# Kernel tuning notes

Hardware: AMD Instinct MI355X
Metric: run time of the kernel (lower is better)

## Reference

```python
import jax, jax.numpy as jnp
import numpy as np

EPS = 1e-8  # torch F.cosine_similarity default eps


def _cos_gram(x):
    # row-normalize with eps-clamped norms, then Gram matrix [N, N]
    norms = jnp.maximum(jnp.linalg.norm(x, axis=1, keepdims=True), EPS)
    xn = x / norms
    return xn @ xn.T


def setup_inputs() -> dict:
    key = jax.random.key(0)
    k1, k2 = jax.random.split(key)
    N, D = 8192, 128
    return {
        "feat_q": jax.random.normal(k1, (N, D), dtype=jnp.float32),
        "feat_k": jax.random.normal(k2, (N, D), dtype=jnp.float32),
    }


def reference(feat_q, feat_k):
    feat_k = jax.lax.stop_gradient(feat_k)  # feat_k.detach()
    N = feat_q.shape[0]
    qsim = _cos_gram(feat_q)  # [N, N]
    ksim = _cos_gram(feat_k)  # [N, N]
    # mean of (qsim - ksim)^2 over all off-diagonal (i != j) pairs
    diff2 = (qsim - ksim) ** 2
    off_diag = ~jnp.eye(N, dtype=bool)
    denom = jnp.asarray(N * (N - 1), dtype=diff2.dtype)
    loss = jnp.sum(jnp.where(off_diag, diff2, 0.0)) / denom
    return loss
```

## Files before the change

kernel.cpp:

```cpp
#include <hip/hip_runtime.h>
#include <hip/hip_bf16.h>

#define NROWS 8192
#define DDIM  128
#define KTOT  256
#define GT_ROWB (NROWS * 2)
#define NKCH  64
#define CHN   (NROWS / NKCH)
#define NPAIR 10
#define GB_BLOCKS 160
#define LDSPAD 260

typedef unsigned short ushort_t;
typedef unsigned int   uint_t;
typedef __attribute__((ext_vector_type(8))) short short8;
typedef __attribute__((ext_vector_type(4))) float floatx4;

#define LDS_PTR(p) ((__attribute__((address_space(3))) void*)(p))
#define GLB_PTR(p) ((const __attribute__((address_space(1))) void*)(p))

static __device__ inline ushort_t f2bf(float f) {
    union { float f; uint_t u; } a; a.f = f;
    uint_t u = a.u + 0x7fffu + ((a.u >> 16) & 1u);
    return (ushort_t)(u >> 16);
}

static __device__ inline void pair_decode(int p, int* ti, int* tj) {
    int i = 0, len = 4;
    while (p >= len) { p -= len; len--; i++; }
    *ti = i; *tj = i + p;
}

__global__ __launch_bounds__(256) void norm_t_kernel(
    const float* __restrict__ q, const float* __restrict__ k,
    ushort_t* __restrict__ Gt, double* acc, uint_t* counter)
{
    __shared__ ushort_t lds[64 * LDSPAD];
    if (blockIdx.x == 0 && threadIdx.x == 0) { *acc = 0.0; *counter = 0u; }
    int w  = threadIdx.x >> 6;
    int l  = threadIdx.x & 63;
    int h  = l >> 5;
    int li = l & 31;

    #pragma unroll
    for (int i = 0; i < 8; ++i) {
        int rl  = w * 16 + 2 * i + h;
        int row = blockIdx.x * 64 + rl;
        {
            float4 v = ((const float4*)(q + (size_t)row * DDIM))[li];
            float ss = v.x * v.x + v.y * v.y + v.z * v.z + v.w * v.w;
            #pragma unroll
            for (int o = 16; o > 0; o >>= 1) ss += __shfl_xor(ss, o, 64);
            float inv = rsqrtf(fmaxf(ss, 1e-16f));
            uint2 p2;
            p2.x = (uint_t)f2bf(v.x * inv) | ((uint_t)f2bf(v.y * inv) << 16);
            p2.y = (uint_t)f2bf(v.z * inv) | ((uint_t)f2bf(v.w * inv) << 16);
            *(uint2*)&lds[rl * LDSPAD + 4 * li] = p2;
        }
        {
            float4 v = ((const float4*)(k + (size_t)row * DDIM))[li];
            float ss = v.x * v.x + v.y * v.y + v.z * v.z + v.w * v.w;
            #pragma unroll
            for (int o = 16; o > 0; o >>= 1) ss += __shfl_xor(ss, o, 64);
            float inv = rsqrtf(fmaxf(ss, 1e-16f));
            uint2 p2;
            p2.x = (uint_t)f2bf(v.x * inv) | ((uint_t)f2bf(v.y * inv) << 16);
            p2.y = (uint_t)f2bf(v.z * inv) | ((uint_t)f2bf(v.w * inv) << 16);
            *(uint2*)&lds[rl * LDSPAD + 128 + 4 * li] = p2;
        }
    }
    __syncthreads();

    int a = threadIdx.x;
    char* gdst = (char*)Gt + (size_t)a * GT_ROWB + (size_t)blockIdx.x * 128;
    #pragma unroll
    for (int g = 0; g < 8; ++g) {
        union { ushort_t u16[8]; uint4 v; } tmp;
        #pragma unroll
        for (int e = 0; e < 8; ++e)
            tmp.u16[e] = lds[(g * 8 + e) * LDSPAD + a];
        *(uint4*)(gdst + g * 16) = tmp.v;
    }
}

__global__ __launch_bounds__(128, 2) void gram_a_kernel(
    const ushort_t* __restrict__ Gt, float* __restrict__ P)
{
    __shared__ ushort_t sA[64 * CHN];
    __shared__ ushort_t sB[64 * CHN];

    int pair = blockIdx.x >> 6;
    int c    = blockIdx.x & 63;
    int ti, tj;
    pair_decode(pair, &ti, &tj);
    int tid = threadIdx.x;

    const char* gA = (const char*)Gt + (size_t)(ti * 64) * GT_ROWB + c * (CHN * 2);
    const char* gB = (const char*)Gt + (size_t)(tj * 64) * GT_ROWB + c * (CHN * 2);

    #pragma unroll
    for (int it = 0; it < 8; ++it) {
        int ch = it * 128 + tid;
        int row = ch >> 4, phys = ch & 15;
        int logical = phys ^ (row & 7);
        __builtin_amdgcn_global_load_lds(GLB_PTR(gA + (size_t)row * GT_ROWB + logical * 16),
                                         LDS_PTR((char*)sA + ch * 16), 16, 0, 0);
    }
    #pragma unroll
    for (int it = 0; it < 8; ++it) {
        int ch = it * 128 + tid;
        int row = ch >> 4, phys = ch & 15;
        int logical = phys ^ (row & 7);
        __builtin_amdgcn_global_load_lds(GLB_PTR(gB + (size_t)row * GT_ROWB + logical * 16),
                                         LDS_PTR((char*)sB + ch * 16), 16, 0, 0);
    }
    __syncthreads();

    int w    = tid >> 6;
    int l    = tid & 63;
    int m    = l & 15;
    int quad = l >> 4;

    floatx4 accC[2][4];
    #pragma unroll
    for (int at = 0; at < 2; ++at)
        #pragma unroll
        for (int bt = 0; bt < 4; ++bt)
            accC[at][bt] = (floatx4){0.f, 0.f, 0.f, 0.f};

    #pragma unroll
    for (int kp = 0; kp < 4; ++kp) {
        short8 af[2], bf[4];
        #pragma unroll
        for (int at = 0; at < 2; ++at) {
            int ra   = w * 32 + at * 16 + m;
            int phys = (kp * 4 + quad) ^ (ra & 7);
            af[at] = *(const short8*)&sA[ra * CHN + phys * 8];
        }
        #pragma unroll
        for (int bt = 0; bt < 4; ++bt) {
            int rb   = bt * 16 + m;
            int phys = (kp * 4 + quad) ^ (rb & 7);
            bf[bt] = *(const short8*)&sB[rb * CHN + phys * 8];
        }
        #pragma unroll
        for (int at = 0; at < 2; ++at)
            #pragma unroll
            for (int bt = 0; bt < 4; ++bt)
                accC[at][bt] = __builtin_amdgcn_mfma_f32_16x16x32_bf16(af[at], bf[bt], accC[at][bt], 0, 0, 0);
    }

    float* pt = P + ((size_t)pair * NKCH + c) * 4096;
    #pragma unroll
    for (int at = 0; at < 2; ++at)
        #pragma unroll
        for (int bt = 0; bt < 4; ++bt)
            #pragma unroll
            for (int r = 0; r < 4; ++r) {
                int row = w * 32 + at * 16 + quad * 4 + r;
                int col = bt * 16 + m;
                pt[row * 64 + col] = accC[at][bt][r];
            }
}

__global__ __launch_bounds__(256) void gram_b_kernel(
    const float* __restrict__ P, double* acc, uint_t* counter, float* out)
{
    __shared__ float wsum[4];
    int e    = blockIdx.x * 256 + threadIdx.x;
    int pair = e >> 12;
    int idx  = e & 4095;

    float s = 0.f;
    #pragma unroll
    for (int c = 0; c < NKCH; ++c)
        s += P[((size_t)pair * NKCH + c) * 4096 + idx];

    int ti, tj;
    pair_decode(pair, &ti, &tj);
    float wgt = ((ti < 2) == (tj < 2)) ? 1.f : -1.f;
    if (ti != tj) wgt *= 2.f;
    float v = wgt * s * s;

    int w = threadIdx.x >> 6, l = threadIdx.x & 63;
    #pragma unroll
    for (int o = 32; o > 0; o >>= 1) v += __shfl_xor(v, o, 64);
    if (l == 0) wsum[w] = v;
    __syncthreads();
    if (threadIdx.x == 0) {
        double t = (double)wsum[0] + (double)wsum[1] + (double)wsum[2] + (double)wsum[3];
        atomicAdd(acc, t);
        __threadfence();
        uint_t old = atomicAdd(counter, 1u);
        if (old == GB_BLOCKS - 1) {
            double total = atomicAdd(acc, 0.0);
            out[0] = (float)(total * (1.0 / ((double)NROWS * (double)(NROWS - 1))));
        }
    }
}

extern "C" void kernel_launch(void* const* d_in, const int* in_sizes, int n_in,
                              void* d_out, int out_size, void* d_ws, size_t ws_size,
                              hipStream_t stream) {
    const float* q = (const float*)d_in[0];
    const float* k = (const float*)d_in[1];
    float* out = (float*)d_out;

    double*   acc = (double*)d_ws;
    uint_t*   cnt = (uint_t*)((char*)d_ws + 64);
    ushort_t* Gt  = (ushort_t*)((char*)d_ws + 256);
    float*    P   = (float*)((char*)d_ws + 256 + (size_t)KTOT * GT_ROWB);

    norm_t_kernel<<<NROWS / 64, 256, 0, stream>>>(q, k, Gt, acc, cnt);
    gram_a_kernel<<<NPAIR * NKCH, 128, 0, stream>>>(Gt, P);
    gram_b_kernel<<<GB_BLOCKS, 256, 0, stream>>>(P, acc, cnt, out);
}
```

Measured before the change: 76.35 us.

## Fuse normalize, Gram and reduce into one cooperative kernel with atomics

Merges the three kernels into a single cooperative launch of 160 blocks that uses grid-wide syncs between phases: normalize/transpose, partial Gram products, and weighted squared reduction. The 64 per-chunk partial tiles are no longer written to a large scratch buffer; each block atomically adds its partial tile into a small 10x4096 accumulator, which removes the big partial write and reread. This saves two kernel launches and that traffic. In exchange it adds grid.sync costs, heavy float atomic contention (64 contributors per element), and nondeterministic float summation order.

```diff
diff --git a/kernel.cpp b/kernel.cpp
--- a/kernel.cpp
+++ b/kernel.cpp
@@ -1,5 +1,8 @@
 #include <hip/hip_runtime.h>
+#include <hip/hip_cooperative_groups.h>
 #include <hip/hip_bf16.h>
+
+namespace cg = cooperative_groups;
 
 #define NROWS 8192
 #define DDIM  128
@@ -8,7 +11,8 @@
 #define NKCH  64
 #define CHN   (NROWS / NKCH)
 #define NPAIR 10
-#define GB_BLOCKS 160
+#define NUNITS (NPAIR * NKCH)
+#define GRID  160
 #define LDSPAD 260
 
 typedef unsigned short ushort_t;
@@ -31,171 +35,186 @@
     *ti = i; *tj = i + p;
 }
 
-__global__ __launch_bounds__(256) void norm_t_kernel(
+__global__ __launch_bounds__(256) void fused_kernel(
     const float* __restrict__ q, const float* __restrict__ k,
-    ushort_t* __restrict__ Gt, double* acc, uint_t* counter)
+    ushort_t* __restrict__ Gt, float* __restrict__ S,
+    double* acc, float* out)
 {
-    __shared__ ushort_t lds[64 * LDSPAD];
-    if (blockIdx.x == 0 && threadIdx.x == 0) { *acc = 0.0; *counter = 0u; }
-    int w  = threadIdx.x >> 6;
-    int l  = threadIdx.x & 63;
-    int h  = l >> 5;
-    int li = l & 31;
-
-    #pragma unroll
-    for (int i = 0; i < 8; ++i) {
-        int rl  = w * 16 + 2 * i + h;
-        int row = blockIdx.x * 64 + rl;
-        {
-            float4 v = ((const float4*)(q + (size_t)row * DDIM))[li];
-            float ss = v.x * v.x + v.y * v.y + v.z * v.z + v.w * v.w;
-            #pragma unroll
-            for (int o = 16; o > 0; o >>= 1) ss += __shfl_xor(ss, o, 64);
-            float inv = rsqrtf(fmaxf(ss, 1e-16f));
-            uint2 p2;
-            p2.x = (uint_t)f2bf(v.x * inv) | ((uint_t)f2bf(v.y * inv) << 16);
-            p2.y = (uint_t)f2bf(v.z * inv) | ((uint_t)f2bf(v.w * inv) << 16);
-            *(uint2*)&lds[rl * LDSPAD + 4 * li] = p2;
-        }
-        {
-            float4 v = ((const float4*)(k + (size_t)row * DDIM))[li];
-            float ss = v.x * v.x + v.y * v.y + v.z * v.z + v.w * v.w;
-            #pragma unroll
-            for (int o = 16; o > 0; o >>= 1) ss += __shfl_xor(ss, o, 64);
-            float inv = rsqrtf(fmaxf(ss, 1e-16f));
-            uint2 p2;
-            p2.x = (uint_t)f2bf(v.x * inv) | ((uint_t)f2bf(v.y * inv) << 16);
-            p2.y = (uint_t)f2bf(v.z * inv) | ((uint_t)f2bf(v.w * inv) << 16);
-            *(uint2*)&lds[rl * LDSPAD + 128 + 4 * li] = p2;
-        }
-    }
-    __syncthreads();
-
-    int a = threadIdx.x;
-    char* gdst = (char*)Gt + (size_t)a * GT_ROWB + (size_t)blockIdx.x * 128;
-    #pragma unroll
-    for (int g = 0; g < 8; ++g) {
-        union { ushort_t u16[8]; uint4 v; } tmp;
-        #pragma unroll
-        for (int e = 0; e < 8; ++e)
-            tmp.u16[e] = lds[(g * 8 + e) * LDSPAD + a];
-        *(uint4*)(gdst + g * 16) = tmp.v;
-    }
-}
-
-__global__ __launch_bounds__(128, 2) void gram_a_kernel(
-    const ushort_t* __restrict__ Gt, float* __restrict__ P)
-{
-    __shared__ ushort_t sA[64 * CHN];
-    __shared__ ushort_t sB[64 * CHN];
-
-    int pair = blockIdx.x >> 6;
-    int c    = blockIdx.x & 63;
-    int ti, tj;
-    pair_decode(pair, &ti, &tj);
+    __shared__ ushort_t lds[32768];
+    cg::grid_group grid = cg::this_grid();
+
     int tid = threadIdx.x;
-
-    const char* gA = (const char*)Gt + (size_t)(ti * 64) * GT_ROWB + c * (CHN * 2);
-    const char* gB = (const char*)Gt + (size_t)(tj * 64) * GT_ROWB + c * (CHN * 2);
-
-    #pragma unroll
-    for (int it = 0; it < 8; ++it) {
-        int ch = it * 128 + tid;
-        int row = ch >> 4, phys = ch & 15;
-        int logical = phys ^ (row & 7);
-        __builtin_amdgcn_global_load_lds(GLB_PTR(gA + (size_t)row * GT_ROWB + logical * 16),
-                                         LDS_PTR((char*)sA + ch * 16), 16, 0, 0);
-    }
-    #pragma unroll
-    for (int it = 0; it < 8; ++it) {
-        int ch = it * 128 + tid;
-        int row = ch >> 4, phys = ch & 15;
-        int logical = phys ^ (row & 7);
-        __builtin_amdgcn_global_load_lds(GLB_PTR(gB + (size_t)row * GT_ROWB + logical * 16),
-                                         LDS_PTR((char*)sB + ch * 16), 16, 0, 0);
-    }
-    __syncthreads();
-
-    int w    = tid >> 6;
-    int l    = tid & 63;
-    int m    = l & 15;
-    int quad = l >> 4;
-
-    floatx4 accC[2][4];
-    #pragma unroll
-    for (int at = 0; at < 2; ++at)
-        #pragma unroll
-        for (int bt = 0; bt < 4; ++bt)
-            accC[at][bt] = (floatx4){0.f, 0.f, 0.f, 0.f};
-
-    #pragma unroll
-    for (int kp = 0; kp < 4; ++kp) {
-        short8 af[2], bf[4];
-        #pragma unroll
-        for (int at = 0; at < 2; ++at) {
-            int ra   = w * 32 + at * 16 + m;
-            int phys = (kp * 4 + quad) ^ (ra & 7);
-            af[at] = *(const short8*)&sA[ra * CHN + phys * 8];
-        }
-        #pragma unroll
-        for (int bt = 0; bt < 4; ++bt) {
-            int rb   = bt * 16 + m;
-            int phys = (kp * 4 + quad) ^ (rb & 7);
-            bf[bt] = *(const short8*)&sB[rb * CHN + phys * 8];
-        }
-        #pragma unroll
-        for (int at = 0; at < 2; ++at)
-            #pragma unroll
-            for (int bt = 0; bt < 4; ++bt)
-                accC[at][bt] = __builtin_amdgcn_mfma_f32_16x16x32_bf16(af[at], bf[bt], accC[at][bt], 0, 0, 0);
-    }
-
-    float* pt = P + ((size_t)pair * NKCH + c) * 4096;
-    #pragma unroll
-    for (int at = 0; at < 2; ++at)
-        #pragma unroll
-        for (int bt = 0; bt < 4; ++bt)
-            #pragma unroll
-            for (int r = 0; r < 4; ++r) {
-                int row = w * 32 + at * 16 + quad * 4 + r;
-                int col = bt * 16 + m;
-                pt[row * 64 + col] = accC[at][bt][r];
-            }
-}
-
-__global__ __launch_bounds__(256) void gram_b_kernel(
-    const float* __restrict__ P, double* acc, uint_t* counter, float* out)
-{
-    __shared__ float wsum[4];
-    int e    = blockIdx.x * 256 + threadIdx.x;
-    int pair = e >> 12;
-    int idx  = e & 4095;
-
-    float s = 0.f;
-    #pragma unroll
-    for (int c = 0; c < NKCH; ++c)
-        s += P[((size_t)pair * NKCH + c) * 4096 + idx];
-
-    int ti, tj;
-    pair_decode(pair, &ti, &tj);
-    float wgt = ((ti < 2) == (tj < 2)) ? 1.f : -1.f;
-    if (ti != tj) wgt *= 2.f;
-    float v = wgt * s * s;
-
-    int w = threadIdx.x >> 6, l = threadIdx.x & 63;
-    #pragma unroll
-    for (int o = 32; o > 0; o >>= 1) v += __shfl_xor(v, o, 64);
-    if (l == 0) wsum[w] = v;
-    __syncthreads();
-    if (threadIdx.x == 0) {
-        double t = (double)wsum[0] + (double)wsum[1] + (double)wsum[2] + (double)wsum[3];
-        atomicAdd(acc, t);
-        __threadfence();
-        uint_t old = atomicAdd(counter, 1u);
-        if (old == GB_BLOCKS - 1) {
-            double total = atomicAdd(acc, 0.0);
-            out[0] = (float)(total * (1.0 / ((double)NROWS * (double)(NROWS - 1))));
-        }
+    int bid = blockIdx.x;
+
+    if (bid < 128) {
+        int w  = tid >> 6;
+        int l  = tid & 63;
+        int h  = l >> 5;
+        int li = l & 31;
+
+        #pragma unroll
+        for (int i = 0; i < 8; ++i) {
+            int rl  = w * 16 + 2 * i + h;
+            int row = bid * 64 + rl;
+            {
+                float4 v = ((const float4*)(q + (size_t)row * DDIM))[li];
+                float ss = v.x * v.x + v.y * v.y + v.z * v.z + v.w * v.w;
+                #pragma unroll
+                for (int o = 16; o > 0; o >>= 1) ss += __shfl_xor(ss, o, 64);
+                float inv = rsqrtf(fmaxf(ss, 1e-16f));
+                uint2 p2;
+                p2.x = (uint_t)f2bf(v.x * inv) | ((uint_t)f2bf(v.y * inv) << 16);
+                p2.y = (uint_t)f2bf(v.z * inv) | ((uint_t)f2bf(v.w * inv) << 16);
+                *(uint2*)&lds[rl * LDSPAD + 4 * li] = p2;
+            }
+            {
+                float4 v = ((const float4*)(k + (size_t)row * DDIM))[li];
+                float ss = v.x * v.x + v.y * v.y + v.z * v.z + v.w * v.w;
+                #pragma unroll
+                for (int o = 16; o > 0; o >>= 1) ss += __shfl_xor(ss, o, 64);
+                float inv = rsqrtf(fmaxf(ss, 1e-16f));
+                uint2 p2;
+                p2.x = (uint_t)f2bf(v.x * inv) | ((uint_t)f2bf(v.y * inv) << 16);
+                p2.y = (uint_t)f2bf(v.z * inv) | ((uint_t)f2bf(v.w * inv) << 16);
+                *(uint2*)&lds[rl * LDSPAD + 128 + 4 * li] = p2;
+            }
+        }
+        __syncthreads();
+
+        int a = tid;
+        char* gdst = (char*)Gt + (size_t)a * GT_ROWB + (size_t)bid * 128;
+        #pragma unroll
+        for (int g = 0; g < 8; ++g) {
+            union { ushort_t u16[8]; uint4 v; } tmp;
+            #pragma unroll
+            for (int e = 0; e < 8; ++e)
+                tmp.u16[e] = lds[(g * 8 + e) * LDSPAD + a];
+            *(uint4*)(gdst + g * 16) = tmp.v;
+        }
+    } else {
+        int base = (bid - 128) * 1280 + tid;
+        #pragma unroll
+        for (int j = 0; j < 5; ++j)
+            S[base + j * 256] = 0.f;
+        if (bid == 128 && tid == 0) *acc = 0.0;
+    }
+    grid.sync();
+
+    {
+        int half   = tid >> 7;
+        int t128   = tid & 127;
+        int sbase  = half * 16384;
+        ushort_t* sA = &lds[sbase];
+        ushort_t* sB = &lds[sbase + 8192];
+
+        int w    = t128 >> 6;
+        int l    = tid & 63;
+        int m    = l & 15;
+        int quad = l >> 4;
+
+        int sb = bid * 2 + half;
+        #pragma unroll
+        for (int rep = 0; rep < 2; ++rep) {
+            int u    = sb + rep * 320;
+            int pair = u >> 6;
+            int c    = u & 63;
+            int ti, tj;
+            pair_decode(pair, &ti, &tj);
+
+            const char* gA = (const char*)Gt + (size_t)(ti * 64) * GT_ROWB + c * (CHN * 2);
+            const char* gB = (const char*)Gt + (size_t)(tj * 64) * GT_ROWB + c * (CHN * 2);
+
+            #pragma unroll
+            for (int it = 0; it < 8; ++it) {
+                int ch = it * 128 + t128;
+                int row = ch >> 4, phys = ch & 15;
+                int logical = phys ^ (row & 7);
+                __builtin_amdgcn_global_load_lds(GLB_PTR(gA + (size_t)row * GT_ROWB + logical * 16),
+                                                 LDS_PTR((char*)sA + ch * 16), 16, 0, 0);
+            }
+            #pragma unroll
+            for (int it = 0; it < 8; ++it) {
+                int ch = it * 128 + t128;
+                int row = ch >> 4, phys = ch & 15;
+                int logical = phys ^ (row & 7);
+                __builtin_amdgcn_global_load_lds(GLB_PTR(gB + (size_t)row * GT_ROWB + logical * 16),
+                                                 LDS_PTR((char*)sB + ch * 16), 16, 0, 0);
+            }
+            __syncthreads();
+
+            floatx4 accC[2][4];
+            #pragma unroll
+            for (int at = 0; at < 2; ++at)
+                #pragma unroll
+                for (int bt = 0; bt < 4; ++bt)
+                    accC[at][bt] = (floatx4){0.f, 0.f, 0.f, 0.f};
+
+            #pragma unroll
+            for (int kp = 0; kp < 4; ++kp) {
+                short8 af[2], bf[4];
+                #pragma unroll
+                for (int at = 0; at < 2; ++at) {
+                    int ra   = w * 32 + at * 16 + m;
+                    int phys = (kp * 4 + quad) ^ (ra & 7);
+                    af[at] = *(const short8*)&sA[ra * CHN + phys * 8];
+                }
+                #pragma unroll
+                for (int bt = 0; bt < 4; ++bt) {
+                    int rb   = bt * 16 + m;
+                    int phys = (kp * 4 + quad) ^ (rb & 7);
+                    bf[bt] = *(const short8*)&sB[rb * CHN + phys * 8];
+                }
+                #pragma unroll
+                for (int at = 0; at < 2; ++at)
+                    #pragma unroll
+                    for (int bt = 0; bt < 4; ++bt)
+                        accC[at][bt] = __builtin_amdgcn_mfma_f32_16x16x32_bf16(af[at], bf[bt], accC[at][bt], 0, 0, 0);
+            }
+
+            float* st = S + pair * 4096;
+            #pragma unroll
+            for (int at = 0; at < 2; ++at)
+                #pragma unroll
+                for (int bt = 0; bt < 4; ++bt)
+                    #pragma unroll
+                    for (int r = 0; r < 4; ++r) {
+                        int row = w * 32 + at * 16 + quad * 4 + r;
+                        int col = bt * 16 + m;
+                        atomicAdd(&st[row * 64 + col], accC[at][bt][r]);
+                    }
+            __syncthreads();
+        }
+    }
+    grid.sync();
+
+    {
+        __shared__ float wsum[4];
+        int e    = bid * 256 + tid;
+        int pair = e >> 12;
+        int idx  = e & 4095;
+
+        float s = S[(size_t)pair * 4096 + idx];
+        int ti, tj;
+        pair_decode(pair, &ti, &tj);
+        float wgt = ((ti < 2) == (tj < 2)) ? 1.f : -1.f;
+        if (ti != tj) wgt *= 2.f;
+        float v = wgt * s * s;
+
+        int w = tid >> 6, l = tid & 63;
+        #pragma unroll
+        for (int o = 32; o > 0; o >>= 1) v += __shfl_xor(v, o, 64);
+        if (l == 0) wsum[w] = v;
+        __syncthreads();
+        if (tid == 0) {
+            double t = (double)wsum[0] + (double)wsum[1] + (double)wsum[2] + (double)wsum[3];
+            atomicAdd(acc, t);
+        }
+    }
+    grid.sync();
+
+    if (bid == 0 && tid == 0) {
+        double total = atomicAdd(acc, 0.0);
+        out[0] = (float)(total * (1.0 / ((double)NROWS * (double)(NROWS - 1))));
     }
 }
 
@@ -207,11 +226,10 @@
     float* out = (float*)d_out;
 
     double*   acc = (double*)d_ws;
-    uint_t*   cnt = (uint_t*)((char*)d_ws + 64);
     ushort_t* Gt  = (ushort_t*)((char*)d_ws + 256);
-    float*    P   = (float*)((char*)d_ws + 256 + (size_t)KTOT * GT_ROWB);
-
-    norm_t_kernel<<<NROWS / 64, 256, 0, stream>>>(q, k, Gt, acc, cnt);
-    gram_a_kernel<<<NPAIR * NKCH, 128, 0, stream>>>(Gt, P);
-    gram_b_kernel<<<GB_BLOCKS, 256, 0, stream>>>(P, acc, cnt, out);
-}
+    float*    S   = (float*)((char*)d_ws + 256 + (size_t)KTOT * GT_ROWB);
+
+    void* args[] = { (void*)&q, (void*)&k, (void*)&Gt, (void*)&S, (void*)&acc, (void*)&out };
+    hipLaunchCooperativeKernel((const void*)fused_kernel, dim3(GRID), dim3(256),
+                               args, 0, stream);
+}
```

After: 143.5 us. 1.88x slower.

## Fuse row normalization and transpose into the partial Gram kernel

Applied to the files above, without the earlier changes.

Removes the separate normalize/transpose kernel and its global bf16 transposed buffer. Each Gram block now reads its 128-row chunk of q or k in fp32, normalizes it, converts to bf16, and transposes it through LDS into the swizzled panel layout before running the MFMA loop. This saves one launch and a global write-plus-read round trip. In exchange, every block redundantly reads and normalizes full 128-wide rows while keeping only half the columns, uses more LDS, and adds extra barriers.

```diff
diff --git a/kernel.cpp b/kernel.cpp
--- a/kernel.cpp
+++ b/kernel.cpp
@@ -3,21 +3,16 @@
 
 #define NROWS 8192
 #define DDIM  128
-#define KTOT  256
-#define GT_ROWB (NROWS * 2)
 #define NKCH  64
 #define CHN   (NROWS / NKCH)
 #define NPAIR 10
 #define GB_BLOCKS 160
-#define LDSPAD 260
+#define NBP   68
 
 typedef unsigned short ushort_t;
 typedef unsigned int   uint_t;
 typedef __attribute__((ext_vector_type(8))) short short8;
 typedef __attribute__((ext_vector_type(4))) float floatx4;
-
-#define LDS_PTR(p) ((__attribute__((address_space(3))) void*)(p))
-#define GLB_PTR(p) ((const __attribute__((address_space(1))) void*)(p))
 
 static __device__ inline ushort_t f2bf(float f) {
     union { float f; uint_t u; } a; a.f = f;
@@ -31,93 +26,68 @@
     *ti = i; *tj = i + p;
 }
 
-__global__ __launch_bounds__(256) void norm_t_kernel(
+__global__ __launch_bounds__(128, 2) void fused_gram_kernel(
     const float* __restrict__ q, const float* __restrict__ k,
-    ushort_t* __restrict__ Gt, double* acc, uint_t* counter)
+    float* __restrict__ P, double* acc, uint_t* counter)
 {
-    __shared__ ushort_t lds[64 * LDSPAD];
-    if (blockIdx.x == 0 && threadIdx.x == 0) { *acc = 0.0; *counter = 0u; }
-    int w  = threadIdx.x >> 6;
-    int l  = threadIdx.x & 63;
-    int h  = l >> 5;
-    int li = l & 31;
-
-    #pragma unroll
-    for (int i = 0; i < 8; ++i) {
-        int rl  = w * 16 + 2 * i + h;
-        int row = blockIdx.x * 64 + rl;
-        {
-            float4 v = ((const float4*)(q + (size_t)row * DDIM))[li];
-            float ss = v.x * v.x + v.y * v.y + v.z * v.z + v.w * v.w;
-            #pragma unroll
-            for (int o = 16; o > 0; o >>= 1) ss += __shfl_xor(ss, o, 64);
-            float inv = rsqrtf(fmaxf(ss, 1e-16f));
-            uint2 p2;
-            p2.x = (uint_t)f2bf(v.x * inv) | ((uint_t)f2bf(v.y * inv) << 16);
-            p2.y = (uint_t)f2bf(v.z * inv) | ((uint_t)f2bf(v.w * inv) << 16);
-            *(uint2*)&lds[rl * LDSPAD + 4 * li] = p2;
-        }
-        {
-            float4 v = ((const float4*)(k + (size_t)row * DDIM))[li];
-            float ss = v.x * v.x + v.y * v.y + v.z * v.z + v.w * v.w;
-            #pragma unroll
-            for (int o = 16; o > 0; o >>= 1) ss += __shfl_xor(ss, o, 64);
-            float inv = rsqrtf(fmaxf(ss, 1e-16f));
-            uint2 p2;
-            p2.x = (uint_t)f2bf(v.x * inv) | ((uint_t)f2bf(v.y * inv) << 16);
-            p2.y = (uint_t)f2bf(v.z * inv) | ((uint_t)f2bf(v.w * inv) << 16);
-            *(uint2*)&lds[rl * LDSPAD + 128 + 4 * li] = p2;
-        }
-    }
-    __syncthreads();
-
-    int a = threadIdx.x;
-    char* gdst = (char*)Gt + (size_t)a * GT_ROWB + (size_t)blockIdx.x * 128;
-    #pragma unroll
-    for (int g = 0; g < 8; ++g) {
-        union { ushort_t u16[8]; uint4 v; } tmp;
-        #pragma unroll
-        for (int e = 0; e < 8; ++e)
-            tmp.u16[e] = lds[(g * 8 + e) * LDSPAD + a];
-        *(uint4*)(gdst + g * 16) = tmp.v;
-    }
-}
-
-__global__ __launch_bounds__(128, 2) void gram_a_kernel(
-    const ushort_t* __restrict__ Gt, float* __restrict__ P)
-{
+    __shared__ ushort_t nbuf[CHN * NBP];
     __shared__ ushort_t sA[64 * CHN];
     __shared__ ushort_t sB[64 * CHN];
+
+    if (blockIdx.x == 0 && threadIdx.x == 0) { *acc = 0.0; *counter = 0u; }
 
     int pair = blockIdx.x >> 6;
     int c    = blockIdx.x & 63;
     int ti, tj;
     pair_decode(pair, &ti, &tj);
+
     int tid = threadIdx.x;
-
-    const char* gA = (const char*)Gt + (size_t)(ti * 64) * GT_ROWB + c * (CHN * 2);
-    const char* gB = (const char*)Gt + (size_t)(tj * 64) * GT_ROWB + c * (CHN * 2);
+    int w   = tid >> 6;
+    int l   = tid & 63;
+    int h   = l >> 5;
+    int li  = l & 31;
 
     #pragma unroll
-    for (int it = 0; it < 8; ++it) {
-        int ch = it * 128 + tid;
-        int row = ch >> 4, phys = ch & 15;
-        int logical = phys ^ (row & 7);
-        __builtin_amdgcn_global_load_lds(GLB_PTR(gA + (size_t)row * GT_ROWB + logical * 16),
-                                         LDS_PTR((char*)sA + ch * 16), 16, 0, 0);
+    for (int p = 0; p < 2; ++p) {
+        int t = p ? tj : ti;
+        const float* src = (t < 2) ? q : k;
+        int half = t & 1;
+        ushort_t* panel = p ? sB : sA;
+
+        #pragma unroll
+        for (int it = 0; it < 32; ++it) {
+            int rl  = it * 4 + w * 2 + h;
+            int row = c * CHN + rl;
+            float4 v = ((const float4*)(src + (size_t)row * DDIM))[li];
+            float ss = v.x * v.x + v.y * v.y + v.z * v.z + v.w * v.w;
+            #pragma unroll
+            for (int o = 16; o > 0; o >>= 1) ss += __shfl_xor(ss, o, 64);
+            float inv = rsqrtf(fmaxf(ss, 1e-16f));
+            int col = 4 * li - 64 * half;
+            if (col >= 0 && col < 64) {
+                uint2 p2;
+                p2.x = (uint_t)f2bf(v.x * inv) | ((uint_t)f2bf(v.y * inv) << 16);
+                p2.y = (uint_t)f2bf(v.z * inv) | ((uint_t)f2bf(v.w * inv) << 16);
+                *(uint2*)&nbuf[rl * NBP + col] = p2;
+            }
+        }
+        __syncthreads();
+
+        int a   = tid & 63;
+        int seg = tid >> 6;
+        #pragma unroll
+        for (int cl = 0; cl < 8; ++cl) {
+            int ch = seg * 8 + cl;
+            union { ushort_t u16[8]; uint4 v; } tmp;
+            #pragma unroll
+            for (int e = 0; e < 8; ++e)
+                tmp.u16[e] = nbuf[(ch * 8 + e) * NBP + a];
+            int slot = ch ^ (a & 7);
+            *(uint4*)&panel[a * CHN + slot * 8] = tmp.v;
+        }
+        __syncthreads();
     }
-    #pragma unroll
-    for (int it = 0; it < 8; ++it) {
-        int ch = it * 128 + tid;
-        int row = ch >> 4, phys = ch & 15;
-        int logical = phys ^ (row & 7);
-        __builtin_amdgcn_global_load_lds(GLB_PTR(gB + (size_t)row * GT_ROWB + logical * 16),
-                                         LDS_PTR((char*)sB + ch * 16), 16, 0, 0);
-    }
-    __syncthreads();
 
-    int w    = tid >> 6;
-    int l    = tid & 63;
     int m    = l & 15;
     int quad = l >> 4;
 
@@ -206,12 +176,10 @@
     const float* k = (const float*)d_in[1];
     float* out = (float*)d_out;
 
-    double*   acc = (double*)d_ws;
-    uint_t*   cnt = (uint_t*)((char*)d_ws + 64);
-    ushort_t* Gt  = (ushort_t*)((char*)d_ws + 256);
-    float*    P   = (float*)((char*)d_ws + 256 + (size_t)KTOT * GT_ROWB);
+    double* acc = (double*)d_ws;
+    uint_t* cnt = (uint_t*)((char*)d_ws + 64);
+    float*  P   = (float*)((char*)d_ws + 256);
 
-    norm_t_kernel<<<NROWS / 64, 256, 0, stream>>>(q, k, Gt, acc, cnt);
-    gram_a_kernel<<<NPAIR * NKCH, 128, 0, stream>>>(Gt, P);
+    fused_gram_kernel<<<NPAIR * NKCH, 128, 0, stream>>>(q, k, P, acc, cnt);
     gram_b_kernel<<<GB_BLOCKS, 256, 0, stream>>>(P, acc, cnt, out);
 }
```

Measured after the change: 94.50 us. 1.24x slower.

## Store transposed features chunk-contiguous so gram loads read contiguous tiles

Applied to the files above, without the earlier changes.

The intermediate transposed bf16 buffer moves from a [256 x 8192] row-major layout to per-chunk blocks [64 chunks][256 rows][128 cols], so each gram_a block's 64x128 tile is a contiguous 16 KB region instead of rows strided by 16 KB. The normalization kernel now handles 32 rows per block and writes transposed elements into a small padded LDS tile with scalar 16-bit stores, then emits 64-byte row segments. This is meant to improve DRAM/cache locality for the tile loads, at the cost of more scalar LDS writes and twice as many normalization blocks.

```diff
diff --git a/kernel.cpp b/kernel.cpp
--- a/kernel.cpp
+++ b/kernel.cpp
@@ -3,13 +3,11 @@
 
 #define NROWS 8192
 #define DDIM  128
-#define KTOT  256
-#define GT_ROWB (NROWS * 2)
 #define NKCH  64
-#define CHN   (NROWS / NKCH)
+#define CHN   128
 #define NPAIR 10
 #define GB_BLOCKS 160
-#define LDSPAD 260
+#define NPAD  38
 
 typedef unsigned short ushort_t;
 typedef unsigned int   uint_t;
@@ -35,27 +33,31 @@
     const float* __restrict__ q, const float* __restrict__ k,
     ushort_t* __restrict__ Gt, double* acc, uint_t* counter)
 {
-    __shared__ ushort_t lds[64 * LDSPAD];
+    __shared__ ushort_t lds[256 * NPAD];
     if (blockIdx.x == 0 && threadIdx.x == 0) { *acc = 0.0; *counter = 0u; }
-    int w  = threadIdx.x >> 6;
-    int l  = threadIdx.x & 63;
-    int h  = l >> 5;
-    int li = l & 31;
-
-    #pragma unroll
-    for (int i = 0; i < 8; ++i) {
-        int rl  = w * 16 + 2 * i + h;
-        int row = blockIdx.x * 64 + rl;
+
+    int b   = blockIdx.x;
+    int c   = b >> 2;
+    int sub = b & 3;
+    int w   = threadIdx.x >> 6;
+    int l   = threadIdx.x & 63;
+    int h   = l >> 5;
+    int li  = l & 31;
+
+    #pragma unroll
+    for (int i = 0; i < 4; ++i) {
+        int rl  = i * 8 + w * 2 + h;
+        int row = b * 32 + rl;
         {
             float4 v = ((const float4*)(q + (size_t)row * DDIM))[li];
             float ss = v.x * v.x + v.y * v.y + v.z * v.z + v.w * v.w;
             #pragma unroll
             for (int o = 16; o > 0; o >>= 1) ss += __shfl_xor(ss, o, 64);
             float inv = rsqrtf(fmaxf(ss, 1e-16f));
-            uint2 p2;
-            p2.x = (uint_t)f2bf(v.x * inv) | ((uint_t)f2bf(v.y * inv) << 16);
-            p2.y = (uint_t)f2bf(v.z * inv) | ((uint_t)f2bf(v.w * inv) << 16);
-            *(uint2*)&lds[rl * LDSPAD + 4 * li] = p2;
+            lds[(4 * li + 0) * NPAD + rl] = f2bf(v.x * inv);
+            lds[(4 * li + 1) * NPAD + rl] = f2bf(v.y * inv);
+            lds[(4 * li + 2) * NPAD + rl] = f2bf(v.z * inv);
+            lds[(4 * li + 3) * NPAD + rl] = f2bf(v.w * inv);
         }
         {
             float4 v = ((const float4*)(k + (size_t)row * DDIM))[li];
@@ -63,24 +65,24 @@
             #pragma unroll
             for (int o = 16; o > 0; o >>= 1) ss += __shfl_xor(ss, o, 64);
             float inv = rsqrtf(fmaxf(ss, 1e-16f));
-            uint2 p2;
-            p2.x = (uint_t)f2bf(v.x * inv) | ((uint_t)f2bf(v.y * inv) << 16);
-            p2.y = (uint_t)f2bf(v.z * inv) | ((uint_t)f2bf(v.w * inv) << 16);
-            *(uint2*)&lds[rl * LDSPAD + 128 + 4 * li] = p2;
+            lds[(128 + 4 * li + 0) * NPAD + rl] = f2bf(v.x * inv);
+            lds[(128 + 4 * li + 1) * NPAD + rl] = f2bf(v.y * inv);
+            lds[(128 + 4 * li + 2) * NPAD + rl] = f2bf(v.z * inv);
+            lds[(128 + 4 * li + 3) * NPAD + rl] = f2bf(v.w * inv);
         }
     }
     __syncthreads();
 
     int a = threadIdx.x;
-    char* gdst = (char*)Gt + (size_t)a * GT_ROWB + (size_t)blockIdx.x * 128;
-    #pragma unroll
-    for (int g = 0; g < 8; ++g) {
-        union { ushort_t u16[8]; uint4 v; } tmp;
-        #pragma unroll
-        for (int e = 0; e < 8; ++e)
-            tmp.u16[e] = lds[(g * 8 + e) * LDSPAD + a];
-        *(uint4*)(gdst + g * 16) = tmp.v;
-    }
+    union { uint_t u32[16]; uint4 v4[4]; } tb;
+    #pragma unroll
+    for (int t = 0; t < 16; ++t)
+        tb.u32[t] = *(const uint_t*)&lds[a * NPAD + 2 * t];
+
+    char* gdst = (char*)Gt + (size_t)(c * 256 + a) * (CHN * 2) + sub * 64;
+    #pragma unroll
+    for (int g = 0; g < 4; ++g)
+        *(uint4*)(gdst + g * 16) = tb.v4[g];
 }
 
 __global__ __launch_bounds__(128, 2) void gram_a_kernel(
@@ -95,15 +97,15 @@
     pair_decode(pair, &ti, &tj);
     int tid = threadIdx.x;
 
-    const char* gA = (const char*)Gt + (size_t)(ti * 64) * GT_ROWB + c * (CHN * 2);
-    const char* gB = (const char*)Gt + (size_t)(tj * 64) * GT_ROWB + c * (CHN * 2);
+    const char* gA = (const char*)Gt + (size_t)(c * 256 + ti * 64) * (CHN * 2);
+    const char* gB = (const char*)Gt + (size_t)(c * 256 + tj * 64) * (CHN * 2);
 
     #pragma unroll
     for (int it = 0; it < 8; ++it) {
         int ch = it * 128 + tid;
         int row = ch >> 4, phys = ch & 15;
         int logical = phys ^ (row & 7);
-        __builtin_amdgcn_global_load_lds(GLB_PTR(gA + (size_t)row * GT_ROWB + logical * 16),
+        __builtin_amdgcn_global_load_lds(GLB_PTR(gA + row * 256 + logical * 16),
                                          LDS_PTR((char*)sA + ch * 16), 16, 0, 0);
     }
     #pragma unroll
@@ -111,7 +113,7 @@
         int ch = it * 128 + tid;
         int row = ch >> 4, phys = ch & 15;
         int logical = phys ^ (row & 7);
-        __builtin_amdgcn_global_load_lds(GLB_PTR(gB + (size_t)row * GT_ROWB + logical * 16),
+        __builtin_amdgcn_global_load_lds(GLB_PTR(gB + row * 256 + logical * 16),
                                          LDS_PTR((char*)sB + ch * 16), 16, 0, 0);
     }
     __syncthreads();
@@ -209,9 +211,9 @@
     double*   acc = (double*)d_ws;
     uint_t*   cnt = (uint_t*)((char*)d_ws + 64);
     ushort_t* Gt  = (ushort_t*)((char*)d_ws + 256);
-    float*    P   = (float*)((char*)d_ws + 256 + (size_t)KTOT * GT_ROWB);
-
-    norm_t_kernel<<<NROWS / 64, 256, 0, stream>>>(q, k, Gt, acc, cnt);
+    float*    P   = (float*)((char*)d_ws + 256 + (size_t)NKCH * 256 * CHN * 2);
+
+    norm_t_kernel<<<NROWS / 32, 256, 0, stream>>>(q, k, Gt, acc, cnt);
     gram_a_kernel<<<NPAIR * NKCH, 128, 0, stream>>>(Gt, P);
     gram_b_kernel<<<GB_BLOCKS, 256, 0, stream>>>(P, acc, cnt, out);
 }
```

Measured after the change: 73.82 us. -3.3%, faster.
